# Performance work log

Measured on AMD Instinct MI355X. Metric: run time of the kernel, lower is better.

## Reference

```python
import jax, jax.numpy as jnp
import numpy as np

B, T, D = 8, 1024, 1024
F = 4 * D  # RWKV channel-mixing hidden size
EPS = 1e-3  # keras LayerNormalization default epsilon


def layer_norm(x, g, b):
    mu = jnp.mean(x, axis=-1, keepdims=True)
    var = jnp.var(x, axis=-1, keepdims=True)
    return (x - mu) * jax.lax.rsqrt(var + EPS) * g + b


def setup_inputs() -> dict:
    key = jax.random.key(0)
    ks = jax.random.split(key, 16)
    s = 0.02
    f32 = jnp.float32
    return {
        "x": jax.random.normal(ks[0], (B, T, D), f32),
        "att_x": jnp.zeros((B, D), f32),
        "att_a": jnp.zeros((B, D), f32),
        "att_b": jnp.zeros((B, D), f32),
        "att_p": jnp.zeros((B, D), f32),
        "ffn_x": jnp.zeros((B, D), f32),
        "ln1_g": jnp.ones((D,), f32),
        "ln1_b": jnp.zeros((D,), f32),
        "ln2_g": jnp.ones((D,), f32),
        "ln2_b": jnp.zeros((D,), f32),
        "tm_mix_k": jax.random.uniform(ks[1], (D,), f32),
        "tm_mix_v": jax.random.uniform(ks[2], (D,), f32),
        "tm_mix_r": jax.random.uniform(ks[3], (D,), f32),
        "tm_decay": jax.random.normal(ks[4], (D,), f32) * 0.1,
        "tm_first": jax.random.normal(ks[5], (D,), f32) * 0.1,
        "Wk": jax.random.normal(ks[6], (D, D), f32) * s,
        "Wv": jax.random.normal(ks[7], (D, D), f32) * s,
        "Wr": jax.random.normal(ks[8], (D, D), f32) * s,
        "Wo": jax.random.normal(ks[9], (D, D), f32) * s,
        "cm_mix_k": jax.random.uniform(ks[10], (D,), f32),
        "cm_mix_r": jax.random.uniform(ks[11], (D,), f32),
        "Ck": jax.random.normal(ks[12], (D, F), f32) * s,
        "Cr": jax.random.normal(ks[13], (D, D), f32) * s,
        "Cv": jax.random.normal(ks[14], (F, D), f32) * s,
    }


def _wkv_scan(k, v, aa, bb, pp, decay, first):
    # k, v: [B, T, D]; states: [B, D]. Numerically-stable RWKV-4 WKV recurrence.
    w = -jnp.exp(decay)  # per-channel decay, always negative

    def step(carry, kv):
        aa, bb, pp = carry
        k_t, v_t = kv
        ww = first + k_t
        p = jnp.maximum(pp, ww)
        e1 = jnp.exp(pp - p)
        e2 = jnp.exp(ww - p)
        wkv = (e1 * aa + e2 * v_t) / (e1 * bb + e2)
        ww2 = pp + w
        p2 = jnp.maximum(ww2, k_t)
        e1b = jnp.exp(ww2 - p2)
        e2b = jnp.exp(k_t - p2)
        return (e1b * aa + e2b * v_t, e1b * bb + e2b, p2), wkv

    kT = jnp.swapaxes(k, 0, 1)  # [T, B, D]
    vT = jnp.swapaxes(v, 0, 1)
    (aa, bb, pp), wkv = jax.lax.scan(step, (aa, bb, pp), (kT, vT))
    return jnp.swapaxes(wkv, 0, 1), aa, bb, pp


def reference(x, att_x, att_a, att_b, att_p, ffn_x,
              ln1_g, ln1_b, ln2_g, ln2_b,
              tm_mix_k, tm_mix_v, tm_mix_r, tm_decay, tm_first,
              Wk, Wv, Wr, Wo, cm_mix_k, cm_mix_r, Ck, Cr, Cv):
    # ---- time mixing (RWKV attention) on ln1(x) ----
    xn = layer_norm(x, ln1_g, ln1_b)  # [B, T, D]
    x_prev = jnp.concatenate([att_x[:, None, :], xn[:, :-1, :]], axis=1)  # token shift
    k = (xn * tm_mix_k + x_prev * (1.0 - tm_mix_k)) @ Wk
    v = (xn * tm_mix_v + x_prev * (1.0 - tm_mix_v)) @ Wv
    r = jax.nn.sigmoid((xn * tm_mix_r + x_prev * (1.0 - tm_mix_r)) @ Wr)
    wkv, aa, bb, pp = _wkv_scan(k, v, att_a, att_b, att_p, tm_decay, tm_first)
    x1 = x + (r * wkv) @ Wo  # residual

    # ---- channel mixing (FFN) on ln2(x1) ----
    xn2 = layer_norm(x1, ln2_g, ln2_b)
    xp = jnp.concatenate([ffn_x[:, None, :], xn2[:, :-1, :]], axis=1)
    kc = jnp.square(jax.nn.relu((xn2 * cm_mix_k + xp * (1.0 - cm_mix_k)) @ Ck))
    rc = jax.nn.sigmoid((xn2 * cm_mix_r + xp * (1.0 - cm_mix_r)) @ Cr)
    out = x1 + rc * (kc @ Cv)

    return (out, xn[:, -1, :], aa, bb, pp, xn2[:, -1, :])
```

## Files before the change

### kernel.cpp

```cpp
#include <hip/hip_runtime.h>

#define TT 1024
#define DD 1024
#define BB 8
#define FF 4096
#define MM (BB * TT)
#define CHL 32
#define NCH (TT / CHL)
#define NCHAN (BB * DD)

typedef unsigned short u16;
typedef unsigned int u32;

typedef __attribute__((ext_vector_type(8))) short short8;
typedef __attribute__((ext_vector_type(4))) float floatx4;

__device__ __forceinline__ u16 f2bf(float f) {
  u32 u = __float_as_uint(f);
  u32 r = (u + 0x7fffu + ((u >> 16) & 1u)) >> 16;
  return (u16)r;
}
__device__ __forceinline__ float bf2f(u16 h) { return __uint_as_float(((u32)h) << 16); }
__device__ __forceinline__ float sigmoidf_(float v) { return 1.0f / (1.0f + __expf(-v)); }

__global__ __launch_bounds__(256) void prologue_kernel(
    const float* __restrict__ x, const float* __restrict__ attx,
    const float* __restrict__ g, const float* __restrict__ be,
    const float* __restrict__ mk, const float* __restrict__ mv, const float* __restrict__ mr,
    u16* __restrict__ xk, u16* __restrict__ xv, u16* __restrict__ xr,
    float* __restrict__ xn_last,
    const float* __restrict__ Wk, const float* __restrict__ Wv, const float* __restrict__ Wr,
    u16* __restrict__ WT4) {
  int id = blockIdx.x;
  int tid = threadIdx.x;
  __shared__ float tile[32][33];
  __shared__ float red[4][4];

  if (id < MM) {
    int row = id;
    int b = row >> 10, t = row & (TT - 1);
    float4 xc = ((const float4*)(x + (size_t)row * DD))[tid];
    float4 xp = (t == 0) ? ((const float4*)(attx + (size_t)b * DD))[tid]
                         : ((const float4*)(x + (size_t)(row - 1) * DD))[tid];
    float sc = xc.x + xc.y + xc.z + xc.w;
    float qc = xc.x * xc.x + xc.y * xc.y + xc.z * xc.z + xc.w * xc.w;
    float sp = xp.x + xp.y + xp.z + xp.w;
    float qp = xp.x * xp.x + xp.y * xp.y + xp.z * xp.z + xp.w * xp.w;
#pragma unroll
    for (int o = 32; o > 0; o >>= 1) {
      sc += __shfl_xor(sc, o); qc += __shfl_xor(qc, o);
      sp += __shfl_xor(sp, o); qp += __shfl_xor(qp, o);
    }
    int lane = tid & 63, wid = tid >> 6;
    if (lane == 0) { red[wid][0] = sc; red[wid][1] = qc; red[wid][2] = sp; red[wid][3] = qp; }
    __syncthreads();
    sc = red[0][0] + red[1][0] + red[2][0] + red[3][0];
    qc = red[0][1] + red[1][1] + red[2][1] + red[3][1];
    sp = red[0][2] + red[1][2] + red[2][2] + red[3][2];
    qp = red[0][3] + red[1][3] + red[2][3] + red[3][3];
    const float inv = 1.0f / (float)DD;
    float muc = sc * inv, varc = qc * inv - muc * muc;
    float rc = rsqrtf(varc + 1e-3f);
    float mup = sp * inv, varp = qp * inv - mup * mup;
    float rp = rsqrtf(varp + 1e-3f);
    float4 gg = ((const float4*)g)[tid];
    float4 bb = ((const float4*)be)[tid];
    float4 k4 = ((const float4*)mk)[tid];
    float4 v4 = ((const float4*)mv)[tid];
    float4 r4 = ((const float4*)mr)[tid];
    float xcv[4] = {xc.x, xc.y, xc.z, xc.w};
    float xpv[4] = {xp.x, xp.y, xp.z, xp.w};
    float gv[4] = {gg.x, gg.y, gg.z, gg.w};
    float bv[4] = {bb.x, bb.y, bb.z, bb.w};
    float kv[4] = {k4.x, k4.y, k4.z, k4.w};
    float vv[4] = {v4.x, v4.y, v4.z, v4.w};
    float rv[4] = {r4.x, r4.y, r4.z, r4.w};
    u16 ok[4], ov[4], orr[4];
    float nc[4];
#pragma unroll
    for (int i = 0; i < 4; i++) {
      nc[i] = (xcv[i] - muc) * rc * gv[i] + bv[i];
      float np = (t == 0) ? xpv[i] : ((xpv[i] - mup) * rp * gv[i] + bv[i]);
      ok[i] = f2bf(nc[i] * kv[i] + np * (1.0f - kv[i]));
      ov[i] = f2bf(nc[i] * vv[i] + np * (1.0f - vv[i]));
      orr[i] = f2bf(nc[i] * rv[i] + np * (1.0f - rv[i]));
    }
    size_t o4 = (size_t)row * (DD / 4) + tid;
    ((ushort4*)xk)[o4] = make_ushort4(ok[0], ok[1], ok[2], ok[3]);
    ((ushort4*)xv)[o4] = make_ushort4(ov[0], ov[1], ov[2], ov[3]);
    ((ushort4*)xr)[o4] = make_ushort4(orr[0], orr[1], orr[2], orr[3]);
    if (t == TT - 1)
      ((float4*)xn_last)[(size_t)b * (DD / 4) + tid] = make_float4(nc[0], nc[1], nc[2], nc[3]);
    return;
  }

  id -= MM;
  int tx = tid & 31, ty = tid >> 5;
  int z = id >> 10, i = id & 1023;
  const float* s3[3] = {Wk, Wv, Wr};
  const float* in = s3[z];
  u16* outp = WT4 + (size_t)z * 1024 * 1024;
  int bx = i & 31, by = i >> 5;
  int n0 = bx * 32, k0 = by * 32;
#pragma unroll
  for (int j = 0; j < 32; j += 8)
    tile[ty + j][tx] = in[(size_t)(k0 + ty + j) * 1024 + (n0 + tx)];
  __syncthreads();
#pragma unroll
  for (int j = 0; j < 32; j += 8)
    outp[(size_t)(n0 + ty + j) * 1024 + (k0 + tx)] = f2bf(tile[tx][ty + j]);
}

__global__ void ln2mix_kernel(const float* __restrict__ x1, const float* __restrict__ ffnx,
                              const float* __restrict__ g, const float* __restrict__ be,
                              const float* __restrict__ cmk, const float* __restrict__ cmr,
                              u16* __restrict__ xk2, u16* __restrict__ xr2,
                              float* __restrict__ xn2_last) {
  int row = blockIdx.x, tid = threadIdx.x;
  int b = row >> 10, t = row & (TT - 1);
  float4 xc = ((const float4*)(x1 + (size_t)row * DD))[tid];
  float4 xp = (t == 0) ? ((const float4*)(ffnx + (size_t)b * DD))[tid]
                       : ((const float4*)(x1 + (size_t)(row - 1) * DD))[tid];
  float sc = xc.x + xc.y + xc.z + xc.w;
  float qc = xc.x * xc.x + xc.y * xc.y + xc.z * xc.z + xc.w * xc.w;
  float sp = xp.x + xp.y + xp.z + xp.w;
  float qp = xp.x * xp.x + xp.y * xp.y + xp.z * xp.z + xp.w * xp.w;
#pragma unroll
  for (int o = 32; o > 0; o >>= 1) {
    sc += __shfl_xor(sc, o); qc += __shfl_xor(qc, o);
    sp += __shfl_xor(sp, o); qp += __shfl_xor(qp, o);
  }
  __shared__ float red[4][4];
  int lane = tid & 63, wid = tid >> 6;
  if (lane == 0) { red[wid][0] = sc; red[wid][1] = qc; red[wid][2] = sp; red[wid][3] = qp; }
  __syncthreads();
  sc = red[0][0] + red[1][0] + red[2][0] + red[3][0];
  qc = red[0][1] + red[1][1] + red[2][1] + red[3][1];
  sp = red[0][2] + red[1][2] + red[2][2] + red[3][2];
  qp = red[0][3] + red[1][3] + red[2][3] + red[3][3];
  const float inv = 1.0f / (float)DD;
  float muc = sc * inv, varc = qc * inv - muc * muc;
  float rc = rsqrtf(varc + 1e-3f);
  float mup = sp * inv, varp = qp * inv - mup * mup;
  float rp = rsqrtf(varp + 1e-3f);
  float4 gg = ((const float4*)g)[tid];
  float4 bb = ((const float4*)be)[tid];
  float4 k4 = ((const float4*)cmk)[tid];
  float4 r4 = ((const float4*)cmr)[tid];
  float xcv[4] = {xc.x, xc.y, xc.z, xc.w};
  float xpv[4] = {xp.x, xp.y, xp.z, xp.w};
  float gv[4] = {gg.x, gg.y, gg.z, gg.w};
  float bv[4] = {bb.x, bb.y, bb.z, bb.w};
  float kv[4] = {k4.x, k4.y, k4.z, k4.w};
  float rv[4] = {r4.x, r4.y, r4.z, r4.w};
  u16 ok[4], orr[4];
  float nc[4];
#pragma unroll
  for (int i = 0; i < 4; i++) {
    nc[i] = (xcv[i] - muc) * rc * gv[i] + bv[i];
    float np = (t == 0) ? xpv[i] : ((xpv[i] - mup) * rp * gv[i] + bv[i]);
    ok[i] = f2bf(nc[i] * kv[i] + np * (1.0f - kv[i]));
    orr[i] = f2bf(nc[i] * rv[i] + np * (1.0f - rv[i]));
  }
  size_t o4 = (size_t)row * (DD / 4) + tid;
  ((ushort4*)xk2)[o4] = make_ushort4(ok[0], ok[1], ok[2], ok[3]);
  ((ushort4*)xr2)[o4] = make_ushort4(orr[0], orr[1], orr[2], orr[3]);
  if (t == TT - 1)
    ((float4*)xn2_last)[(size_t)b * (DD / 4) + tid] = make_float4(nc[0], nc[1], nc[2], nc[3]);
}

__global__ void wkv_chunk_sum(const u16* __restrict__ K, const u16* __restrict__ V,
                              const float* __restrict__ decay,
                              float* __restrict__ sa, float* __restrict__ sb,
                              float* __restrict__ ps) {
  int f = blockIdx.x * 256 + threadIdx.x;
  int d = f & (DD - 1);
  int bc = f >> 10;
  int b = bc & (BB - 1);
  int chunk = bc >> 3;
  float w = -__expf(decay[d]);
  const u16* kp = K + ((size_t)(b * TT + chunk * CHL)) * DD + d;
  const u16* vp = V + ((size_t)(b * TT + chunk * CHL)) * DD + d;
  float aa = 0.0f, bb = 0.0f, pp = -1e30f;
#pragma unroll
  for (int j = 0; j < CHL; j++) {
    float kt = bf2f(kp[(size_t)j * DD]);
    float vt = bf2f(vp[(size_t)j * DD]);
    float ww2 = pp + w;
    float p2 = fmaxf(ww2, kt);
    float e1 = __expf(ww2 - p2);
    float e2 = __expf(kt - p2);
    aa = e1 * aa + e2 * vt;
    bb = e1 * bb + e2;
    pp = p2;
  }
  int ch = b * DD + d;
  size_t s = (size_t)chunk * NCHAN + ch;
  sa[s] = aa; sb[s] = bb; ps[s] = pp;
}

__global__ void wkv_chunk_scan(const float* __restrict__ sa, const float* __restrict__ sb,
                               const float* __restrict__ ps, const float* __restrict__ decay,
                               const float* __restrict__ aa0, const float* __restrict__ bb0,
                               const float* __restrict__ pp0,
                               float* __restrict__ pa, float* __restrict__ pb,
                               float* __restrict__ ppx,
                               float* __restrict__ aa_out, float* __restrict__ bb_out,
                               float* __restrict__ pp_out) {
  int ch = blockIdx.x * 256 + threadIdx.x;
  int d = ch & (DD - 1);
  float w = -__expf(decay[d]);
  float wL = (float)CHL * w;
  float aa = aa0[ch], bb = bb0[ch], pp = pp0[ch];
  float lsa[NCH], lsb[NCH], lps[NCH];
#pragma unroll
  for (int j = 0; j < NCH; j++) {
    size_t s = (size_t)j * NCHAN + ch;
    lsa[j] = sa[s]; lsb[j] = sb[s]; lps[j] = ps[s];
  }
#pragma unroll
  for (int j = 0; j < NCH; j++) {
    size_t s = (size_t)j * NCHAN + ch;
    pa[s] = aa; pb[s] = bb; ppx[s] = pp;
    float pw = pp + wL;
    float pn = fmaxf(pw, lps[j]);
    float e1 = __expf(pw - pn);
    float e2 = __expf(lps[j] - pn);
    aa = e1 * aa + e2 * lsa[j];
    bb = e1 * bb + e2 * lsb[j];
    pp = pn;
  }
  aa_out[ch] = aa; bb_out[ch] = bb; pp_out[ch] = pp;
}

__global__ void wkv_chunk_out(const u16* __restrict__ K, const u16* __restrict__ V,
                              const u16* __restrict__ sigr, const float* __restrict__ decay,
                              const float* __restrict__ first,
                              const float* __restrict__ pa, const float* __restrict__ pb,
                              const float* __restrict__ ppx, u16* __restrict__ rm) {
  int f = blockIdx.x * 256 + threadIdx.x;
  int d = f & (DD - 1);
  int bc = f >> 10;
  int b = bc & (BB - 1);
  int chunk = bc >> 3;
  float w = -__expf(decay[d]);
  float u = first[d];
  int ch = b * DD + d;
  size_t s = (size_t)chunk * NCHAN + ch;
  float aa = pa[s], bb = pb[s], pp = ppx[s];
  size_t base = ((size_t)(b * TT + chunk * CHL)) * DD + d;
  const u16* kp = K + base;
  const u16* vp = V + base;
  const u16* rp = sigr + base;
  u16* op = rm + base;
#pragma unroll
  for (int j = 0; j < CHL; j++) {
    float kt = bf2f(kp[(size_t)j * DD]);
    float vt = bf2f(vp[(size_t)j * DD]);
    float ww = u + kt;
    float p = fmaxf(pp, ww);
    float e1 = __expf(pp - p);
    float e2 = __expf(ww - p);
    float wkv = __fdividef(e1 * aa + e2 * vt, e1 * bb + e2);
    op[(size_t)j * DD] = f2bf(bf2f(rp[(size_t)j * DD]) * wkv);
    float ww2 = pp + w;
    float p2 = fmaxf(ww2, kt);
    float e1b = __expf(ww2 - p2);
    float e2b = __expf(kt - p2);
    aa = e1b * aa + e2b * vt;
    bb = e1b * bb + e2b;
    pp = p2;
  }
}


template <int MODE>
__launch_bounds__(256, 4)
__global__ void gemm_bt(const u16* __restrict__ A0, const u16* __restrict__ A1,
                        const u16* __restrict__ BT0,
                        const float* R1, const u16* R2,
                        void* C0, void* C1, int M, int N, int K,
                        const float* TW0, const float* TW1, const float* TW2, const float* TW3,
                        u16* TO0, u16* TO1, u16* TO2, u16* TO3) {
  __shared__ u16 lA[128 * 64];
  __shared__ u16 lB[128 * 64];
  int tid = threadIdx.x;

  if (MODE == 5 && blockIdx.z >= 3) {
    int id = (blockIdx.z - 3) * 512 + blockIdx.y * gridDim.x + blockIdx.x;
    float* tile = (float*)lA;
    int tx = tid & 31, ty = tid >> 5;
    const float* in;
    u16* outp;
    int K2, N2, bx2, by2;
    if (id < 1024) {
      in = TW0; outp = TO0; K2 = 1024; N2 = 1024; bx2 = id & 31; by2 = id >> 5;
    } else if (id < 2048) {
      int i = id - 1024;
      in = TW1; outp = TO1; K2 = 1024; N2 = 1024; bx2 = i & 31; by2 = i >> 5;
    } else if (id < 6144) {
      int i = id - 2048;
      in = TW2; outp = TO2; K2 = 1024; N2 = 4096; bx2 = i & 127; by2 = i >> 7;
    } else {
      int i = id - 6144;
      in = TW3; outp = TO3; K2 = 4096; N2 = 1024; bx2 = i & 31; by2 = i >> 5;
    }
    int n0 = bx2 * 32, k0 = by2 * 32;
#pragma unroll
    for (int j = 0; j < 32; j += 8)
      tile[(ty + j) * 33 + tx] = in[(size_t)(k0 + ty + j) * N2 + (n0 + tx)];
    __syncthreads();
#pragma unroll
    for (int j = 0; j < 32; j += 8)
      outp[(size_t)(n0 + ty + j) * K2 + (k0 + tx)] = f2bf(tile[tx * 33 + (ty + j)]);
    return;
  }

  int lane = tid & 63;
  int wid = tid >> 6;
  int wy = wid >> 1, wx = wid & 1;

  const u16* A = A0;
  const u16* BT = BT0;
  void* Cout = C0;
  if (MODE == 5) {
    int z = blockIdx.z;
    A = A0 + (size_t)z * M * K;
    BT = BT0 + (size_t)z * N * K;
    Cout = (void*)((u16*)C0 + (size_t)z * M * N);
  }

  int bx = blockIdx.x, by = blockIdx.y;
  {
    int flat = by * gridDim.x + bx;
    int j = flat >> 3;
    by = (flat & 7) * 8 + (j & 7);
    bx = j >> 3;
  }
  int m0 = by * 128, n0 = bx * 128;

  bool isCr = false;
  if (MODE == 6) {
    isCr = (bx >= 32);
    A = isCr ? A1 : A0;
  }

  int rlo = lane & 15;
  int rr = tid >> 3;
  int cc = ((tid & 7) - rr) & 7;
  const u16* gA = A + (size_t)(m0 + rr) * K + cc * 8;
  const u16* gB = BT + (size_t)(n0 + rr) * K + cc * 8;
  u16* ldsA = lA + wid * 512;
  u16* ldsB = lB + wid * 512;
  size_t qstep = (size_t)32 * K;

  floatx4 acc[4][4];
#pragma unroll
  for (int mi = 0; mi < 4; mi++)
#pragma unroll
    for (int ni = 0; ni < 4; ni++)
#pragma unroll
      for (int e = 0; e < 4; e++) acc[mi][ni][e] = 0.0f;

  for (int kt = 0; kt < K; kt += 64) {
    __syncthreads();
#pragma unroll
    for (int q = 0; q < 4; q++) {
      __builtin_amdgcn_global_load_lds(gA + q * qstep + kt, ldsA + q * 2048, 16, 0, 0);
      __builtin_amdgcn_global_load_lds(gB + q * qstep + kt, ldsB + q * 2048, 16, 0, 0);
    }
    __syncthreads();
    short8 af[2][4], bfr[2][4];
#pragma unroll
    for (int s = 0; s < 2; s++) {
      int cbase = s * 4 + (lane >> 4);
#pragma unroll
      for (int mi = 0; mi < 4; mi++) {
        int row = wy * 64 + mi * 16 + rlo;
        af[s][mi] = *(const short8*)&lA[row * 64 + (((cbase + row) & 7) << 3)];
      }
#pragma unroll
      for (int ni = 0; ni < 4; ni++) {
        int row = wx * 64 + ni * 16 + rlo;
        bfr[s][ni] = *(const short8*)&lB[row * 64 + (((cbase + row) & 7) << 3)];
      }
    }
#pragma unroll
    for (int s = 0; s < 2; s++)
#pragma unroll
      for (int mi = 0; mi < 4; mi++)
#pragma unroll
        for (int ni = 0; ni < 4; ni++)
          acc[mi][ni] =
              __builtin_amdgcn_mfma_f32_16x16x32_bf16(af[s][mi], bfr[s][ni], acc[mi][ni], 0, 0, 0);
  }

  int rbase = (lane >> 4) * 4;
#pragma unroll
  for (int mi = 0; mi < 4; mi++) {
#pragma unroll
    for (int ni = 0; ni < 4; ni++) {
#pragma unroll
      for (int r = 0; r < 4; r++) {
        int row = m0 + wy * 64 + mi * 16 + rbase + r;
        int col = n0 + wx * 64 + ni * 16 + rlo;
        float v = acc[mi][ni][r];
        if (MODE == 6) {
          if (!isCr) {
            float tpos = fmaxf(v, 0.0f);
            ((u16*)C0)[(size_t)row * 4096 + col] = f2bf(tpos * tpos);
          } else {
            ((u16*)C1)[(size_t)row * 1024 + (col - 4096)] = f2bf(sigmoidf_(v));
          }
        } else {
          size_t idx = (size_t)row * N + col;
          if (MODE == 3) {
            ((float*)Cout)[idx] = v + R1[idx];
          } else if (MODE == 4) {
            ((float*)Cout)[idx] = R1[idx] + bf2f(R2[idx]) * v;
          } else if (MODE == 5) {
            ((u16*)Cout)[idx] = (blockIdx.z == 2) ? f2bf(sigmoidf_(v)) : f2bf(v);
          }
        }
      }
    }
  }
}

extern "C" void kernel_launch(void* const* d_in, const int* in_sizes, int n_in,
                              void* d_out, int out_size, void* d_ws, size_t ws_size,
                              hipStream_t stream) {
  const float* x    = (const float*)d_in[0];
  const float* attx = (const float*)d_in[1];
  const float* aa0  = (const float*)d_in[2];
  const float* bb0  = (const float*)d_in[3];
  const float* pp0  = (const float*)d_in[4];
  const float* ffnx = (const float*)d_in[5];
  const float* ln1g = (const float*)d_in[6];
  const float* ln1b = (const float*)d_in[7];
  const float* ln2g = (const float*)d_in[8];
  const float* ln2b = (const float*)d_in[9];
  const float* mk   = (const float*)d_in[10];
  const float* mv   = (const float*)d_in[11];
  const float* mr   = (const float*)d_in[12];
  const float* decay= (const float*)d_in[13];
  const float* first= (const float*)d_in[14];
  const float* Wk   = (const float*)d_in[15];
  const float* Wv   = (const float*)d_in[16];
  const float* Wr   = (const float*)d_in[17];
  const float* Wo   = (const float*)d_in[18];
  const float* cmk  = (const float*)d_in[19];
  const float* cmr  = (const float*)d_in[20];
  const float* Ck   = (const float*)d_in[21];
  const float* Cr   = (const float*)d_in[22];
  const float* Cv   = (const float*)d_in[23];

  float* out      = (float*)d_out;
  float* xn_last  = out + (size_t)BB * TT * DD;
  float* aa_out   = xn_last + BB * DD;
  float* bb_out   = aa_out + BB * DD;
  float* pp_out   = bb_out + BB * DD;
  float* xn2_last = pp_out + BB * DD;
  float* x1 = out;

  char* ws = (char*)d_ws;
  const size_t MB = 1024ull * 1024ull;
  u16* WT4   = (u16*)(ws + 0 * MB);
  u16* WkT   = WT4;
  u16* WoT   = WT4 + 3u * 1024 * 1024;
  u16* CkCrT = (u16*)(ws + 8 * MB);
  u16* CrTd  = CkCrT + (size_t)4096 * 1024;
  u16* CvT   = (u16*)(ws + 18 * MB);
  u16* xk    = (u16*)(ws + 26 * MB);
  u16* xv    = (u16*)(ws + 42 * MB);
  u16* xr    = (u16*)(ws + 58 * MB);
  u16* kbuf  = (u16*)(ws + 74 * MB);
  u16* vbuf  = (u16*)(ws + 90 * MB);
  u16* sigr  = (u16*)(ws + 106 * MB);
  float* sab = (float*)(ws + 122 * MB);
  float* sbb = (float*)(ws + 123 * MB);
  float* psb = (float*)(ws + 124 * MB);
  float* pab = (float*)(ws + 125 * MB);
  float* pbb = (float*)(ws + 126 * MB);
  float* ppb = (float*)(ws + 127 * MB);
  u16* rmb   = (u16*)(ws + 26 * MB);
  u16* xk2   = (u16*)(ws + 26 * MB);
  u16* xr2   = (u16*)(ws + 42 * MB);
  u16* sigr2 = (u16*)(ws + 58 * MB);
  u16* kc    = (u16*)(ws + 74 * MB);

  prologue_kernel<<<MM + 3072, 256, 0, stream>>>(
      x, attx, ln1g, ln1b, mk, mv, mr, xk, xv, xr, xn_last, Wk, Wv, Wr, WT4);

  gemm_bt<5><<<dim3(8, 64, 23), 256, 0, stream>>>(
      xk, nullptr, WkT, nullptr, nullptr, kbuf, nullptr, MM, 1024, 1024,
      Wo, Cr, Ck, Cv, WoT, CrTd, CkCrT, CvT);

  wkv_chunk_sum<<<NCHAN * NCH / 256, 256, 0, stream>>>(kbuf, vbuf, decay, sab, sbb, psb);
  wkv_chunk_scan<<<NCHAN / 256, 256, 0, stream>>>(sab, sbb, psb, decay, aa0, bb0, pp0,
                                                  pab, pbb, ppb, aa_out, bb_out, pp_out);
  wkv_chunk_out<<<NCHAN * NCH / 256, 256, 0, stream>>>(kbuf, vbuf, sigr, decay, first,
                                                       pab, pbb, ppb, rmb);

  gemm_bt<3><<<dim3(8, 64), 256, 0, stream>>>(rmb, nullptr, WoT, x, nullptr,
                                              x1, nullptr, MM, 1024, 1024,
                                              nullptr, nullptr, nullptr, nullptr,
                                              nullptr, nullptr, nullptr, nullptr);

  ln2mix_kernel<<<MM, 256, 0, stream>>>(x1, ffnx, ln2g, ln2b, cmk, cmr, xk2, xr2, xn2_last);

  gemm_bt<6><<<dim3(40, 64), 256, 0, stream>>>(xk2, xr2, CkCrT, nullptr, nullptr,
                                               kc, sigr2, MM, 5120, 1024,
                                               nullptr, nullptr, nullptr, nullptr,
                                               nullptr, nullptr, nullptr, nullptr);

  gemm_bt<4><<<dim3(8, 64), 256, 0, stream>>>(kc, nullptr, CvT, x1, sigr2,
                                              out, nullptr, MM, 1024, 4096,
                                              nullptr, nullptr, nullptr, nullptr,
                                              nullptr, nullptr, nullptr, nullptr);
}
```

Measured before the change: 496.2 us.

## Fuse WKV chunk scan into output kernel and use 64-row GEMM tiles for N=1024

```diff
diff --git a/kernel.cpp b/kernel.cpp
--- a/kernel.cpp
+++ b/kernel.cpp
@@ -199,60 +199,43 @@
   sa[s] = aa; sb[s] = bb; ps[s] = pp;
 }
 
-__global__ void wkv_chunk_scan(const float* __restrict__ sa, const float* __restrict__ sb,
-                               const float* __restrict__ ps, const float* __restrict__ decay,
-                               const float* __restrict__ aa0, const float* __restrict__ bb0,
-                               const float* __restrict__ pp0,
-                               float* __restrict__ pa, float* __restrict__ pb,
-                               float* __restrict__ ppx,
-                               float* __restrict__ aa_out, float* __restrict__ bb_out,
-                               float* __restrict__ pp_out) {
-  int ch = blockIdx.x * 256 + threadIdx.x;
-  int d = ch & (DD - 1);
-  float w = -__expf(decay[d]);
-  float wL = (float)CHL * w;
-  float aa = aa0[ch], bb = bb0[ch], pp = pp0[ch];
-  float lsa[NCH], lsb[NCH], lps[NCH];
-#pragma unroll
-  for (int j = 0; j < NCH; j++) {
-    size_t s = (size_t)j * NCHAN + ch;
-    lsa[j] = sa[s]; lsb[j] = sb[s]; lps[j] = ps[s];
-  }
-#pragma unroll
-  for (int j = 0; j < NCH; j++) {
-    size_t s = (size_t)j * NCHAN + ch;
-    pa[s] = aa; pb[s] = bb; ppx[s] = pp;
-    float pw = pp + wL;
-    float pn = fmaxf(pw, lps[j]);
-    float e1 = __expf(pw - pn);
-    float e2 = __expf(lps[j] - pn);
-    aa = e1 * aa + e2 * lsa[j];
-    bb = e1 * bb + e2 * lsb[j];
-    pp = pn;
-  }
-  aa_out[ch] = aa; bb_out[ch] = bb; pp_out[ch] = pp;
-}
-
-__global__ void wkv_chunk_out(const u16* __restrict__ K, const u16* __restrict__ V,
-                              const u16* __restrict__ sigr, const float* __restrict__ decay,
-                              const float* __restrict__ first,
-                              const float* __restrict__ pa, const float* __restrict__ pb,
-                              const float* __restrict__ ppx, u16* __restrict__ rm) {
+__global__ void wkv_scan_out(const u16* __restrict__ K, const u16* __restrict__ V,
+                             const u16* __restrict__ sigr, const float* __restrict__ decay,
+                             const float* __restrict__ first,
+                             const float* __restrict__ aa0, const float* __restrict__ bb0,
+                             const float* __restrict__ pp0,
+                             const float* __restrict__ sa, const float* __restrict__ sb,
+                             const float* __restrict__ ps, u16* __restrict__ rm,
+                             float* __restrict__ aa_out, float* __restrict__ bb_out,
+                             float* __restrict__ pp_out) {
   int f = blockIdx.x * 256 + threadIdx.x;
   int d = f & (DD - 1);
   int bc = f >> 10;
   int b = bc & (BB - 1);
   int chunk = bc >> 3;
+  int ch = b * DD + d;
   float w = -__expf(decay[d]);
-  float u = first[d];
-  int ch = b * DD + d;
-  size_t s = (size_t)chunk * NCHAN + ch;
-  float aa = pa[s], bb = pb[s], pp = ppx[s];
+  float wL = (float)CHL * w;
+
+  float aa = aa0[ch], bb = bb0[ch], pp = pp0[ch];
+  for (int j = 0; j < chunk; j++) {
+    size_t s = (size_t)j * NCHAN + ch;
+    float lsa = sa[s], lsb = sb[s], lps = ps[s];
+    float pw = pp + wL;
+    float pn = fmaxf(pw, lps);
+    float e1 = __expf(pw - pn);
+    float e2 = __expf(lps - pn);
+    aa = e1 * aa + e2 * lsa;
+    bb = e1 * bb + e2 * lsb;
+    pp = pn;
+  }
+
   size_t base = ((size_t)(b * TT + chunk * CHL)) * DD + d;
   const u16* kp = K + base;
   const u16* vp = V + base;
   const u16* rp = sigr + base;
   u16* op = rm + base;
+  float u = first[d];
 #pragma unroll
   for (int j = 0; j < CHL; j++) {
     float kt = bf2f(kp[(size_t)j * DD]);
@@ -271,6 +254,7 @@
     bb = e1b * bb + e2b;
     pp = p2;
   }
+  if (chunk == NCH - 1) { aa_out[ch] = aa; bb_out[ch] = bb; pp_out[ch] = pp; }
 }
 
 
@@ -278,7 +262,6 @@
 __launch_bounds__(256, 4)
 __global__ void gemm_bt(const u16* __restrict__ A0, const u16* __restrict__ A1,
                         const u16* __restrict__ BT0,
-                        const float* R1, const u16* R2,
                         void* C0, void* C1, int M, int N, int K,
                         const float* TW0, const float* TW1, const float* TW2, const float* TW3,
                         u16* TO0, u16* TO1, u16* TO2, u16* TO3) {
@@ -412,15 +395,100 @@
           } else {
             ((u16*)C1)[(size_t)row * 1024 + (col - 4096)] = f2bf(sigmoidf_(v));
           }
+        } else if (MODE == 5) {
+          ((u16*)Cout)[(size_t)row * N + col] = (blockIdx.z == 2) ? f2bf(sigmoidf_(v)) : f2bf(v);
+        }
+      }
+    }
+  }
+}
+
+template <int MODE>
+__launch_bounds__(256, 4)
+__global__ void gemm_bt64(const u16* __restrict__ A0, const u16* __restrict__ BT0,
+                          const float* R1, const u16* R2,
+                          void* C0, int M, int N, int K) {
+  __shared__ u16 lA[64 * 64];
+  __shared__ u16 lB[128 * 64];
+  int tid = threadIdx.x;
+  int lane = tid & 63;
+  int wid = tid >> 6;
+
+  int bx = blockIdx.x, by = blockIdx.y;
+  {
+    int flat = by * gridDim.x + bx;
+    int j = flat >> 3;
+    by = (flat & 7) * 16 + (j & 15);
+    bx = j >> 4;
+  }
+  int m0 = by * 64, n0 = bx * 128;
+
+  int rlo = lane & 15;
+  int rr = tid >> 3;
+  int cc = ((tid & 7) - rr) & 7;
+  const u16* gA = A0 + (size_t)(m0 + rr) * K + cc * 8;
+  const u16* gB = BT0 + (size_t)(n0 + rr) * K + cc * 8;
+  u16* ldsA = lA + wid * 512;
+  u16* ldsB = lB + wid * 512;
+  size_t qstep = (size_t)32 * K;
+
+  floatx4 acc[4][2];
+#pragma unroll
+  for (int mi = 0; mi < 4; mi++)
+#pragma unroll
+    for (int ni = 0; ni < 2; ni++)
+#pragma unroll
+      for (int e = 0; e < 4; e++) acc[mi][ni][e] = 0.0f;
+
+  for (int kt = 0; kt < K; kt += 64) {
+    __syncthreads();
+#pragma unroll
+    for (int q = 0; q < 2; q++)
+      __builtin_amdgcn_global_load_lds(gA + q * qstep + kt, ldsA + q * 2048, 16, 0, 0);
+#pragma unroll
+    for (int q = 0; q < 4; q++)
+      __builtin_amdgcn_global_load_lds(gB + q * qstep + kt, ldsB + q * 2048, 16, 0, 0);
+    __syncthreads();
+    short8 af[2][4], bfr[2][2];
+#pragma unroll
+    for (int s = 0; s < 2; s++) {
+      int cbase = s * 4 + (lane >> 4);
+#pragma unroll
+      for (int mi = 0; mi < 4; mi++) {
+        int row = mi * 16 + rlo;
+        af[s][mi] = *(const short8*)&lA[row * 64 + (((cbase + row) & 7) << 3)];
+      }
+#pragma unroll
+      for (int ni = 0; ni < 2; ni++) {
+        int row = wid * 32 + ni * 16 + rlo;
+        bfr[s][ni] = *(const short8*)&lB[row * 64 + (((cbase + row) & 7) << 3)];
+      }
+    }
+#pragma unroll
+    for (int s = 0; s < 2; s++)
+#pragma unroll
+      for (int mi = 0; mi < 4; mi++)
+#pragma unroll
+        for (int ni = 0; ni < 2; ni++)
+          acc[mi][ni] =
+              __builtin_amdgcn_mfma_f32_16x16x32_bf16(af[s][mi], bfr[s][ni], acc[mi][ni], 0, 0, 0);
+  }
+
+  int rbase = (lane >> 4) * 4;
+#pragma unroll
+  for (int mi = 0; mi < 4; mi++) {
+#pragma unroll
+    for (int ni = 0; ni < 2; ni++) {
+#pragma unroll
+      for (int r = 0; r < 4; r++) {
+        int row = m0 + mi * 16 + rbase + r;
+        int col = n0 + wid * 32 + ni * 16 + rlo;
+        size_t idx = (size_t)row * N + col;
+        float v = acc[mi][ni][r];
+        if (MODE == 3) {
+          ((float*)C0)[idx] = v + R1[idx];
         } else {
-          size_t idx = (size_t)row * N + col;
-          if (MODE == 3) {
-            ((float*)Cout)[idx] = v + R1[idx];
-          } else if (MODE == 4) {
-            ((float*)Cout)[idx] = R1[idx] + bf2f(R2[idx]) * v;
-          } else if (MODE == 5) {
-            ((u16*)Cout)[idx] = (blockIdx.z == 2) ? f2bf(sigmoidf_(v)) : f2bf(v);
-          }
+          ((float*)C0)[idx] = R1[idx] + bf2f(R2[idx]) * v;
         }
       }
     }
@@ -480,9 +548,6 @@
   float* sab = (float*)(ws + 122 * MB);
   float* sbb = (float*)(ws + 123 * MB);
   float* psb = (float*)(ws + 124 * MB);
-  float* pab = (float*)(ws + 125 * MB);
-  float* pbb = (float*)(ws + 126 * MB);
-  float* ppb = (float*)(ws + 127 * MB);
   u16* rmb   = (u16*)(ws + 26 * MB);
   u16* xk2   = (u16*)(ws + 26 * MB);
   u16* xr2   = (u16*)(ws + 42 * MB);
@@ -493,29 +558,21 @@
       x, attx, ln1g, ln1b, mk, mv, mr, xk, xv, xr, xn_last, Wk, Wv, Wr, WT4);
 
   gemm_bt<5><<<dim3(8, 64, 23), 256, 0, stream>>>(
-      xk, nullptr, WkT, nullptr, nullptr, kbuf, nullptr, MM, 1024, 1024,
+      xk, nullptr, WkT, kbuf, nullptr, MM, 1024, 1024,
       Wo, Cr, Ck, Cv, WoT, CrTd, CkCrT, CvT);
 
   wkv_chunk_sum<<<NCHAN * NCH / 256, 256, 0, stream>>>(kbuf, vbuf, decay, sab, sbb, psb);
-  wkv_chunk_scan<<<NCHAN / 256, 256, 0, stream>>>(sab, sbb, psb, decay, aa0, bb0, pp0,
-                                                  pab, pbb, ppb, aa_out, bb_out, pp_out);
-  wkv_chunk_out<<<NCHAN * NCH / 256, 256, 0, stream>>>(kbuf, vbuf, sigr, decay, first,
-                                                       pab, pbb, ppb, rmb);
-
-  gemm_bt<3><<<dim3(8, 64), 256, 0, stream>>>(rmb, nullptr, WoT, x, nullptr,
-                                              x1, nullptr, MM, 1024, 1024,
-                                              nullptr, nullptr, nullptr, nullptr,
-                                              nullptr, nullptr, nullptr, nullptr);
+  wkv_scan_out<<<NCHAN * NCH / 256, 256, 0, stream>>>(kbuf, vbuf, sigr, decay, first,
+                                                      aa0, bb0, pp0, sab, sbb, psb, rmb,
+                                                      aa_out, bb_out, pp_out);
+
+  gemm_bt64<3><<<dim3(8, 128), 256, 0, stream>>>(rmb, WoT, x, nullptr, x1, MM, 1024, 1024);
 
   ln2mix_kernel<<<MM, 256, 0, stream>>>(x1, ffnx, ln2g, ln2b, cmk, cmr, xk2, xr2, xn2_last);
 
-  gemm_bt<6><<<dim3(40, 64), 256, 0, stream>>>(xk2, xr2, CkCrT, nullptr, nullptr,
-                                               kc, sigr2, MM, 5120, 1024,
+  gemm_bt<6><<<dim3(40, 64), 256, 0, stream>>>(xk2, xr2, CkCrT, kc, sigr2, MM, 5120, 1024,
                                                nullptr, nullptr, nullptr, nullptr,
                                                nullptr, nullptr, nullptr, nullptr);
 
-  gemm_bt<4><<<dim3(8, 64), 256, 0, stream>>>(kc, nullptr, CvT, x1, sigr2,
-                                              out, nullptr, MM, 1024, 4096,
-                                              nullptr, nullptr, nullptr, nullptr,
-                                              nullptr, nullptr, nullptr, nullptr);
-}
+  gemm_bt64<4><<<dim3(8, 128), 256, 0, stream>>>(kc, CvT, x1, sigr2, out, MM, 1024, 4096);
+}
```

Result: faster. 477.9 us (-3.7%).
